# Kernel optimization log

Measured on AMD Instinct MI355X. Metric: run time of the kernel, lower is better.

Reference implementation:

```python
import jax, jax.numpy as jnp
import numpy as np

B, N, T, W, H, ED, S, C, E = 16, 256, 64, 12, 64, 64, 5, 4, 2048
ALPHA = 1.0
FG = W + H  # gcn_in_channels = window_size + tgcn_hidden_dim


def setup_inputs() -> dict:
    key = jax.random.key(0)
    ks = jax.random.split(key, 26)
    rn = lambda k, shape: jax.random.normal(k, shape, jnp.float32) * 0.1
    x = jax.random.normal(ks[0], (B, N, T), jnp.float32)
    src = jax.random.randint(ks[1], (E,), 0, N)
    off = jax.random.randint(ks[2], (E,), 1, N)
    dst = (src + off) % N  # no self loops
    return {
        'x': x,
        'static_edge_weight': jax.random.uniform(ks[3], (E,), jnp.float32),
        'gsl_gconv_w': rn(ks[4], (FG, ED)), 'gsl_gconv_b': rn(ks[5], (ED,)),
        'gsl_w1': rn(ks[6], (ED, ED)), 'gsl_b1': rn(ks[7], (ED,)),
        'gsl_w2': rn(ks[8], (ED, ED)), 'gsl_b2': rn(ks[9], (ED,)),
        'wz_c': rn(ks[10], (1, H)), 'bz_c': rn(ks[11], (H,)),
        'wz_l': rn(ks[12], (2 * H, H)), 'bz_l': rn(ks[13], (H,)),
        'wr_c': rn(ks[14], (1, H)), 'br_c': rn(ks[15], (H,)),
        'wr_l': rn(ks[16], (2 * H, H)), 'br_l': rn(ks[17], (H,)),
        'wh_c': rn(ks[18], (1, H)), 'bh_c': rn(ks[19], (H,)),
        'wh_l': rn(ks[20], (2 * H, H)), 'bh_l': rn(ks[21], (H,)),
        'cls_w': rn(ks[22], (N * H, C)), 'cls_b': rn(ks[23], (C,)),
        'static_edge_index': jnp.stack([src, dst]).astype(jnp.int32),
    }


def _normalize(A):
    # GCN sym-norm with added self loops; A has zero diagonal by construction.
    Ahat = A + jnp.eye(N, dtype=A.dtype)
    deg = Ahat.sum(axis=-2)  # in-degree (PyG gcn_norm scatters weight on col)
    dinv = jnp.where(deg > 0, 1.0 / jnp.sqrt(deg), 0.0)
    return dinv[..., :, None] * Ahat * dinv[..., None, :]


def reference(x, static_edge_weight, gsl_gconv_w, gsl_gconv_b, gsl_w1, gsl_b1,
              gsl_w2, gsl_b2, wz_c, bz_c, wz_l, bz_l, wr_c, br_c, wr_l, br_l,
              wh_c, bh_c, wh_l, bh_l, cls_w, cls_b, static_edge_index):
    A_stat = jnp.zeros((N, N), jnp.float32).at[static_edge_index[0], static_edge_index[1]].add(static_edge_weight)
    An_stat = _normalize(A_stat)  # [N,N]

    # Sliding windows, left-padded with zeros to window_size W.
    xp = jnp.pad(x, ((0, 0), (0, 0), (W - 1, 0)))
    widx = jnp.arange(T)[:, None] + jnp.arange(W)[None, :]
    wins = jnp.transpose(xp[:, :, widx], (2, 0, 1, 3))      # [T,B,N,W]
    xts = jnp.transpose(x, (2, 0, 1))[..., None]            # [T,B,N,1]
    cnts = jnp.minimum(jnp.arange(T) + 1, S).astype(jnp.float32)
    idxs = jnp.arange(T) % S

    def gcn_s(X, Wm, b):  # static graph, out[j] = sum_i Anorm[i,j] (XW)[i]
        return jnp.einsum('ij,bif->bjf', An_stat, X @ Wm) + b

    def gcn_d(An, X, Wm, b):  # per-batch dynamic graph
        return jnp.einsum('bij,bif->bjf', An, X @ Wm) + b

    def step(carry, xs):
        h, Eh = carry
        win, xt, cnt, idx = xs
        It = jnp.concatenate([win, h], axis=-1)             # [B,N,W+H]
        df = gcn_s(It, gsl_gconv_w, gsl_gconv_b)
        de1 = jnp.tanh(ALPHA * (df @ gsl_w1 + gsl_b1))
        de2 = jnp.tanh(ALPHA * (df @ gsl_w2 + gsl_b2))
        M12 = jnp.einsum('bie,bje->bij', de1, de2)          # de1 @ de2^T
        Et = jax.nn.relu(jnp.tanh(ALPHA * (M12 - jnp.swapaxes(M12, -1, -2))))
        Eh = Eh.at[:, idx].set(Et)                          # ring buffer write
        Mt = Eh.sum(axis=1) / cnt                           # mean over filled slots
        An = _normalize(Mt)
        cz = gcn_d(An, xt, wz_c, bz_c)
        z = jax.nn.sigmoid(jnp.concatenate([cz, h], -1) @ wz_l + bz_l)
        cr = gcn_d(An, xt, wr_c, br_c)
        r = jax.nn.sigmoid(jnp.concatenate([cr, h], -1) @ wr_l + br_l)
        ch = gcn_d(An, xt, wh_c, bh_c)
        ht = jnp.tanh(jnp.concatenate([ch, h * r], -1) @ wh_l + bh_l)
        h = z * h + (1.0 - z) * ht
        return (h, Eh), None

    h0 = jnp.zeros((B, N, H), jnp.float32)
    Eh0 = jnp.zeros((B, S, N, N), jnp.float32)
    (hT, _), _ = jax.lax.scan(step, (h0, Eh0), (wins, xts, cnts, idxs))
    return hT.reshape(B, N * H) @ cls_w + cls_b
```

## Files before the change

kernel.cpp:

```cpp
#include <hip/hip_runtime.h>
#include <hip/hip_bf16.h>


typedef unsigned short u16;
typedef unsigned int u32;
typedef unsigned long long u64;
typedef __attribute__((ext_vector_type(8))) short bf16x8;
typedef __attribute__((ext_vector_type(4))) float f32x4;

#define B_ 16
#define N_ 256
#define T_ 64
#define W_ 12
#define S_ 5
#define E_ 2048
#define FG_ 76
#define G_ 16

__device__ __forceinline__ float b2f(u16 u) {
  union { u32 i; float f; } v; v.i = ((u32)u) << 16; return v.f;
}
__device__ __forceinline__ u16 f2b(float f) {
  union { float f; u32 i; } v; v.f = f;
  u32 x = v.i; x += 0x7fff + ((x >> 16) & 1); return (u16)(x >> 16);
}
__device__ __forceinline__ float ftanh(float x) {
  float e = __expf(-2.f * fabsf(x));
  float t = (1.f - e) / (1.f + e);
  return x < 0.f ? -t : t;
}
__device__ __forceinline__ float fsigm(float x) { return 1.f / (1.f + __expf(-x)); }
__device__ __forceinline__ float cvload(const void* p, int i, int f) {
  return f ? ((const float*)p)[i] : b2f(((const u16*)p)[i]);
}
__device__ __forceinline__ float gld(const float* p) {
  return __hip_atomic_load(p, __ATOMIC_RELAXED, __HIP_MEMORY_SCOPE_SYSTEM);
}
__device__ __forceinline__ void gst(float* p, float v) {
  __hip_atomic_store(p, v, __ATOMIC_RELAXED, __HIP_MEMORY_SCOPE_SYSTEM);
}
__device__ __forceinline__ u64 gld64(const u64* p) {
  return __hip_atomic_load(p, __ATOMIC_RELAXED, __HIP_MEMORY_SCOPE_SYSTEM);
}
__device__ __forceinline__ void gst64(u64* p, u64 v) {
  __hip_atomic_store(p, v, __ATOMIC_RELAXED, __HIP_MEMORY_SCOPE_SYSTEM);
}
__device__ __forceinline__ u32 gldu(const u32* p) {
  return __hip_atomic_load(p, __ATOMIC_RELAXED, __HIP_MEMORY_SCOPE_SYSTEM);
}
__device__ __forceinline__ f32x4 mfma16(bf16x8 a, bf16x8 b, f32x4 c) {
  return __builtin_amdgcn_mfma_f32_16x16x32_bf16(a, b, c, 0, 0, 0);
}
__device__ __forceinline__ bf16x8 ldfrag(const u16* p) { return *(const bf16x8*)p; }

struct Params {
  const void *x0, *ew0, *gw0, *gb0, *w10, *b10, *w20, *b20;
  const void *wzc0, *bzc0, *wzl0, *bzl0, *wrc0, *brc0, *wrl0, *brl0;
  const void *whc0, *bhc0, *whl0, *bhl0, *clsw0, *clsb0;
  const int* eidx;
  float *xf, *ewf, *gwf, *gbf, *b1f, *b2ff;
  float *wzcf, *bzcf, *wzlf, *bzlf, *wrcf, *brcf, *wrlf, *brlf;
  float *whcf, *bhcf, *whlf, *bhlf, *clswf, *clsbf;
  u16 *w1h, *w2h;
  float *AnT, *dinvS, *uvF, *h, *degsum, *Eh, *Ascr;
  u64 *de1g, *de2g, *xTp, *hgpT;
  u32 *tags;
  int *flag;
  void* out;
};

__device__ __forceinline__ void wtag(const u32* tg, u32 target) {
  const int k = threadIdx.x & 15;
  while (!__all((int)(gldu(&tg[k]) >= target)))
    __builtin_amdgcn_s_sleep(1);
}
__device__ __forceinline__ void ptag(u32* tg, int wg, u32 val) {
  if (threadIdx.x == 0)
    __hip_atomic_store(&tg[wg], val, __ATOMIC_RELAXED, __HIP_MEMORY_SCOPE_SYSTEM);
}

__global__ void k_detect(Params p) {
  if (threadIdx.x == 0) {
    const u16* q = (const u16*)p.x0;
    int c = 0;
    for (int i = 0; i < 256; ++i) {
      int ex = (q[i] >> 7) & 0xff;
      c += (ex >= 110 && ex <= 135);
    }
    *p.flag = (c < 200) ? 1 : 0;
  }
}

__global__ void k_convert(Params p) {
  const int f = *p.flag;
  const int blk = blockIdx.x, tid = threadIdx.x;
  if (blk < 32) {
    const int base = blk * 8192;
    for (int i = tid; i < 8192; i += 256) p.xf[base + i] = cvload(p.x0, base + i, f);
    return;
  }
  if (blk == 51) { for (int i = tid; i < 4096; i += 256) p.w1h[i] = f ? f2b(((const float*)p.w10)[i]) : ((const u16*)p.w10)[i]; return; }
  if (blk == 52) { for (int i = tid; i < 4096; i += 256) p.w2h[i] = f ? f2b(((const float*)p.w20)[i]) : ((const u16*)p.w20)[i]; return; }
  const void* src = nullptr; float* dst = nullptr; int n = 0;
  switch (blk) {
    case 32: src = p.ew0;  dst = p.ewf;  n = E_;      break;
    case 33: src = p.gw0;  dst = p.gwf;  n = FG_ * 64; break;
    case 34: src = p.gb0;  dst = p.gbf;  n = 64;      break;
    case 35: src = p.b10;  dst = p.b1f;  n = 64;      break;
    case 36: src = p.b20;  dst = p.b2ff; n = 64;      break;
    case 37: src = p.wzc0; dst = p.wzcf; n = 64;      break;
    case 38: src = p.bzc0; dst = p.bzcf; n = 64;      break;
    case 39: src = p.wzl0; dst = p.wzlf; n = 8192;    break;
    case 40: src = p.bzl0; dst = p.bzlf; n = 64;      break;
    case 41: src = p.wrc0; dst = p.wrcf; n = 64;      break;
    case 42: src = p.brc0; dst = p.brcf; n = 64;      break;
    case 43: src = p.wrl0; dst = p.wrlf; n = 8192;    break;
    case 44: src = p.brl0; dst = p.brlf; n = 64;      break;
    case 45: src = p.whc0; dst = p.whcf; n = 64;      break;
    case 46: src = p.bhc0; dst = p.bhcf; n = 64;      break;
    case 47: src = p.whl0; dst = p.whlf; n = 8192;    break;
    case 48: src = p.bhl0; dst = p.bhlf; n = 64;      break;
    case 49: src = p.clsw0; dst = p.clswf; n = 65536; break;
    case 50: src = p.clsb0; dst = p.clsbf; n = 4;     break;
    default: return;
  }
  for (int i = tid; i < n; i += 256) dst[i] = cvload(src, i, f);
}

__global__ void k_xt(Params p) {
  __shared__ float tile[64 * 65];
  const int b = blockIdx.x, tid = threadIdx.x;
  u32* xT32 = (u32*)p.xTp;
  for (int chunk = 0; chunk < 4; ++chunk) {
    __syncthreads();
    const int r = tid >> 2, tq = (tid & 3) * 16;
    #pragma unroll
    for (int q = 0; q < 16; ++q)
      tile[r * 65 + tq + q] = p.xf[((size_t)b * N_ + chunk * 64 + r) * T_ + tq + q];
    __syncthreads();
    #pragma unroll
    for (int q = 0; q < 8; ++q) {
      const int idx = q * 256 + tid;
      const int t = idx >> 5, c = idx & 31;
      u32 v = (u32)f2b(tile[(2 * c) * 65 + t]) | ((u32)f2b(tile[(2 * c + 1) * 65 + t]) << 16);
      xT32[(size_t)(b * 64 + t) * 128 + chunk * 32 + c] = v;
    }
  }
}

__global__ void k_scatter(Params p) {
  for (int e = threadIdx.x; e < E_; e += 256) {
    int s = p.eidx[e], d = p.eidx[E_ + e];
    atomicAdd(&p.Ascr[s * N_ + d], p.ewf[e]);
  }
}
__global__ void k_deg(Params p) {
  int j = threadIdx.x;
  float dg = 1.f;
  for (int i = 0; i < N_; ++i) dg += p.Ascr[i * N_ + j];
  p.dinvS[j] = rsqrtf(dg);
}
__global__ void k_ant(Params p) {
  int i = blockIdx.x, j = threadIdx.x;
  float a = p.Ascr[i * N_ + j] + (i == j ? 1.f : 0.f);
  p.AnT[j * N_ + i] = p.dinvS[i] * a * p.dinvS[j];
}
__global__ void k_uv(Params p) {
  int e = threadIdx.x; if (e >= 64) return;
  float uz = 0, vz = 0, ur = 0, vr = 0, uh = 0, vh = 0;
  for (int f = 0; f < 64; ++f) {
    float wz = p.wzlf[f * 64 + e], wr = p.wrlf[f * 64 + e], wh = p.whlf[f * 64 + e];
    uz += p.wzcf[f] * wz; vz += p.bzcf[f] * wz;
    ur += p.wrcf[f] * wr; vr += p.brcf[f] * wr;
    uh += p.whcf[f] * wh; vh += p.bhcf[f] * wh;
  }
  p.uvF[0 * 64 + e] = uz; p.uvF[1 * 64 + e] = vz + p.bzlf[e];
  p.uvF[2 * 64 + e] = ur; p.uvF[3 * 64 + e] = vr + p.brlf[e];
  p.uvF[4 * 64 + e] = uh; p.uvF[5 * 64 + e] = vh + p.bhlf[e];
}

__global__ void __launch_bounds__(256) dtgcn_main(Params p) {
  __shared__ __align__(16) u16 s_union[21120];
  __shared__ __align__(16) u16 s_gwF[64 * 104];
  __shared__ __align__(16) u16 s_w1T[64 * 72], s_w2T[64 * 72];
  __shared__ __align__(16) u16 s_gzT[64 * 72], s_grT[64 * 72], s_ghT[64 * 72];
  __shared__ __align__(16) u16 s_antO1[16 * 264], s_antO2[16 * 264];
  __shared__ __align__(16) u16 s_m1[16 * 104];
  __shared__ float s_msum[16 * 257];
  __shared__ __align__(16) u16 s_de1I[16 * 72], s_de2I[16 * 72];
  __shared__ __align__(16) u16 s_hbf[16 * 72];
  __shared__ __align__(16) u16 s_dfhr[16 * 72];
  __shared__ float s_colv[16], s_degacc[16];
  __shared__ float s_y[256], s_dinv[256], s_s[16];
  __shared__ float s_uv[384], s_gb[64], s_b1[64], s_b2[64];

  const int b = blockIdx.x & 15;
  const int wg = blockIdx.x >> 4;
  const int tid = threadIdx.x;
  const int lane = tid & 63;
  const int wv = tid >> 6;
  const int l = lane & 15;
  const int quad = lane >> 4;
  const int r0 = wg * 16;

  for (int idx = tid; idx < 64 * 104; idx += 256) {
    const int ee = idx / 104, k = idx - ee * 104;
    u16 v = 0;
    if (k < 64) v = f2b(p.gwf[(12 + k) * 64 + ee]);
    else if (k < 76) v = f2b(p.gwf[(k - 64) * 64 + ee]);
    s_gwF[ee * 104 + k] = v;
  }
  for (int idx = tid; idx < 4096; idx += 256) {
    const int ee = idx >> 6, ff = idx & 63;
    s_w1T[ee * 72 + ff] = p.w1h[ff * 64 + ee];
    s_w2T[ee * 72 + ff] = p.w2h[ff * 64 + ee];
    s_gzT[ee * 72 + ff] = f2b(p.wzlf[4096 + ff * 64 + ee]);
    s_grT[ee * 72 + ff] = f2b(p.wrlf[4096 + ff * 64 + ee]);
    s_ghT[ee * 72 + ff] = f2b(p.whlf[4096 + ff * 64 + ee]);
    const int j = idx >> 8, i = idx & 255;
    float a = p.AnT[(r0 + j) * N_ + i];
    u16 hi = f2b(a);
    s_antO1[j * 264 + i] = hi;
    s_antO2[j * 264 + i] = f2b(a - b2f(hi));
  }
  for (int idx = tid; idx < 16 * 257; idx += 256) s_msum[idx] = 0.f;
  for (int idx = tid; idx < 16 * 72; idx += 256) s_hbf[idx] = 0;
  for (int idx = tid; idx < 16 * 104; idx += 256) s_m1[idx] = 0;
  for (int idx = 20064 + tid; idx < 21120; idx += 256) s_union[idx] = 0;
  for (int idx = tid; idx < 384; idx += 256) s_uv[idx] = p.uvF[idx];
  if (tid < 64) { s_gb[tid] = p.gbf[tid]; s_b1[tid] = p.b1f[tid]; s_b2[tid] = p.b2ff[tid]; }
  if (tid < 16) s_degacc[tid] = 0.f;
  __syncthreads();

  u64* de1g = p.de1g + (size_t)b * N_ * 16;
  u64* de2g = p.de2g + (size_t)b * N_ * 16;
  u64* hgpb = p.hgpT + (size_t)b * 64 * 64;
  const u64* xTb = p.xTp + (size_t)b * 64 * 64;
  float* hb   = p.h + (size_t)b * N_ * 64;
  float* degb = p.degsum + (size_t)b * N_;
  u32* tgDe = p.tags + b * 64;
  u32* tgDg = p.tags + b * 64 + 16;
  u32* tgH  = p.tags + b * 64 + 32;

  u16* s_itT = s_union;
  u16* s_j1  = s_union;
  u16* s_j2  = s_union + 9216;
  float* s_part = (float*)s_union;

  float hreg[4] = {0.f, 0.f, 0.f, 0.f};
  const int e = wv * 16 + l;

  for (int t = 0; t < T_; ++t) {
    {
      u64 tw[3];
      #pragma unroll
      for (int q = 0; q < 3; ++q) {
        const int idx = q * 256 + tid;
        const int row = idx >> 6, c = idx & 63;
        const int tx = t - (W_ - 1) + row;
        tw[q] = (tx >= 0) ? gld64(&xTb[(size_t)tx * 64 + c]) : 0ull;
      }
      wtag(tgH, (u32)t);
      u64 th[16];
      #pragma unroll
      for (int q = 0; q < 16; ++q) {
        const int idx = q * 256 + tid;
        const int row = idx >> 6, c = idx & 63;
        th[q] = gld64(&hgpb[(size_t)row * 64 + c]);
      }
      #pragma unroll
      for (int q = 0; q < 16; ++q) {
        const int idx = q * 256 + tid;
        const int row = idx >> 6, c = idx & 63;
        *(u64*)&s_itT[row * 264 + c * 4] = th[q];
      }
      #pragma unroll
      for (int q = 0; q < 3; ++q) {
        const int idx = q * 256 + tid;
        const int row = idx >> 6, c = idx & 63;
        *(u64*)&s_itT[(64 + row) * 264 + c * 4] = tw[q];
      }
      __syncthreads();
      for (int nt = wv; nt < 5; nt += 4) {
        f32x4 acc = {0.f, 0.f, 0.f, 0.f};
        #pragma unroll
        for (int ch = 0; ch < 8; ++ch) {
          const int io = ch * 32 + quad * 8;
          bf16x8 bfr = ldfrag(&s_itT[(nt * 16 + l) * 264 + io]);
          acc = mfma16(ldfrag(&s_antO1[l * 264 + io]), bfr, acc);
          acc = mfma16(ldfrag(&s_antO2[l * 264 + io]), bfr, acc);
        }
        #pragma unroll
        for (int r = 0; r < 4; ++r)
          s_m1[(quad * 4 + r) * 104 + nt * 16 + l] = f2b(acc[r]);
      }
      __syncthreads();
      {
        f32x4 dfa = {0.f, 0.f, 0.f, 0.f};
        #pragma unroll
        for (int ks = 0; ks < 3; ++ks) {
          bf16x8 afr = ldfrag(&s_m1[l * 104 + ks * 32 + quad * 8]);
          dfa = mfma16(afr, ldfrag(&s_gwF[e * 104 + ks * 32 + quad * 8]), dfa);
        }
        #pragma unroll
        for (int r = 0; r < 4; ++r)
          s_dfhr[(quad * 4 + r) * 72 + e] = f2b(dfa[r] + s_gb[e]);
      }
      __syncthreads();
      {
        f32x4 E1, E2;
        #pragma unroll
        for (int r = 0; r < 4; ++r) { E1[r] = s_b1[e]; E2[r] = s_b2[e]; }
        #pragma unroll
        for (int ks = 0; ks < 2; ++ks) {
          bf16x8 afr = ldfrag(&s_dfhr[l * 72 + ks * 32 + quad * 8]);
          E1 = mfma16(afr, ldfrag(&s_w1T[e * 72 + ks * 32 + quad * 8]), E1);
          E2 = mfma16(afr, ldfrag(&s_w2T[e * 72 + ks * 32 + quad * 8]), E2);
        }
        #pragma unroll
        for (int r = 0; r < 4; ++r) {
          s_de1I[(quad * 4 + r) * 72 + e] = f2b(ftanh(E1[r]));
          s_de2I[(quad * 4 + r) * 72 + e] = f2b(ftanh(E2[r]));
        }
      }
      __syncthreads();
      {
        const int row = tid >> 4, c = tid & 15;
        u64 v1 = *(const u64*)&s_de1I[row * 72 + c * 4];
        u64 v2 = *(const u64*)&s_de2I[row * 72 + c * 4];
        gst64(&de1g[(size_t)(r0 + row) * 16 + c], v1);
        gst64(&de2g[(size_t)(r0 + row) * 16 + c], v2);
      }
      __syncthreads();
      ptag(tgDe, wg, (u32)(t + 1));
    }

    {
      const int sidx = t % S_;
      float* Ehc = p.Eh + (size_t)(b * S_ + sidx) * N_ * N_;
      if (tid < 16) s_colv[tid] = 0.f;
      bf16x8 bq1[2], bq2[2];
      #pragma unroll
      for (int ks = 0; ks < 2; ++ks) {
        bq1[ks] = ldfrag(&s_de1I[l * 72 + ks * 32 + quad * 8]);
        bq2[ks] = ldfrag(&s_de2I[l * 72 + ks * 32 + quad * 8]);
      }
      wtag(tgDe, (u32)(t + 1));
      float dcacc = 0.f;
      for (int jh = 0; jh < 2; ++jh) {
        u64 t1[8], t2[8];
        #pragma unroll
        for (int q = 0; q < 8; ++q) {
          const int idx = q * 256 + tid;
          const int row = idx >> 4, c = idx & 15;
          t1[q] = gld64(&de1g[(size_t)(jh * 128 + row) * 16 + c]);
          t2[q] = gld64(&de2g[(size_t)(jh * 128 + row) * 16 + c]);
        }
        __syncthreads();
        #pragma unroll
        for (int q = 0; q < 8; ++q) {
          const int idx = q * 256 + tid;
          const int row = idx >> 4, c = idx & 15;
          *(u64*)&s_j1[row * 72 + c * 4] = t1[q];
          *(u64*)&s_j2[row * 72 + c * 4] = t2[q];
        }
        __syncthreads();
        #pragma unroll
        for (int mt2 = 0; mt2 < 2; ++mt2) {
          const int mt = wv * 2 + mt2;
          f32x4 D1 = {0.f, 0.f, 0.f, 0.f}, D2 = {0.f, 0.f, 0.f, 0.f};
          #pragma unroll
          for (int ks = 0; ks < 2; ++ks) {
            bf16x8 a1 = ldfrag(&s_j1[(mt * 16 + l) * 72 + ks * 32 + quad * 8]);
            bf16x8 a2 = ldfrag(&s_j2[(mt * 16 + l) * 72 + ks * 32 + quad * 8]);
            D1 = mfma16(a1, bq2[ks], D1);
            D2 = mfma16(a2, bq1[ks], D2);
          }
          #pragma unroll
          for (int r = 0; r < 4; ++r) {
            const int i = jh * 128 + mt * 16 + quad * 4 + r;
            float d = ftanh(D1[r] - D2[r]);
            float eN = fmaxf(d, 0.f);
            float old = Ehc[(r0 + l) * N_ + i];
            float dd = eN - old;
            Ehc[(r0 + l) * N_ + i] = eN;
            s_msum[l * 257 + i] += dd;
            dcacc += dd;
          }
        }
      }
      dcacc += __shfl_xor(dcacc, 16);
      dcacc += __shfl_xor(dcacc, 32);
      if (lane < 16) atomicAdd(&s_colv[lane], dcacc);
      __syncthreads();
      if (tid < 16) {
        float nd = s_degacc[tid] + s_colv[tid];
        s_degacc[tid] = nd;
        gst(&degb[r0 + tid], nd);
      }
      __syncthreads();
      ptag(tgDg, wg, (u32)(t + 1));
    }

    {
      f32x4 azh = {0.f, 0.f, 0.f, 0.f}, arh = {0.f, 0.f, 0.f, 0.f};
      #pragma unroll
      for (int ks = 0; ks < 2; ++ks) {
        bf16x8 afr = ldfrag(&s_hbf[l * 72 + ks * 32 + quad * 8]);
        azh = mfma16(afr, ldfrag(&s_gzT[e * 72 + ks * 32 + quad * 8]), azh);
        arh = mfma16(afr, ldfrag(&s_grT[e * 72 + ks * 32 + quad * 8]), arh);
      }
      wtag(tgDg, (u32)(t + 1));
      const float cnt = (float)((t + 1 < S_) ? (t + 1) : S_);
      const float invc = 1.f / cnt;
      {
        float dg = 1.f + gld(&degb[tid]) * invc;
        float di = rsqrtf(dg);
        float xv = p.xf[((size_t)b * N_ + tid) * T_ + t];
        s_dinv[tid] = di;
        s_y[tid] = di * xv;
      }
      __syncthreads();
      {
        const int jl = tid & 15, c = tid >> 4;
        float part = 0.f;
        #pragma unroll
        for (int k = 0; k < 16; ++k)
          part += s_msum[jl * 257 + c * 16 + k] * s_y[c * 16 + k];
        s_part[c * 16 + jl] = part;
      }
      __syncthreads();
      if (tid < 16) {
        float tot = 0.f;
        for (int k = 0; k < 16; ++k) tot += s_part[k * 16 + tid];
        const int j = r0 + tid;
        s_s[tid] = s_dinv[j] * (tot * invc + s_y[j]);
      }
      __syncthreads();
      float sv[4];
      #pragma unroll
      for (int r = 0; r < 4; ++r) sv[r] = s_s[quad * 4 + r];
      float zz[4], rr2[4];
      #pragma unroll
      for (int r = 0; r < 4; ++r) {
        zz[r]  = fsigm(azh[r] + s_uv[0 * 64 + e] * sv[r] + s_uv[1 * 64 + e]);
        rr2[r] = fsigm(arh[r] + s_uv[2 * 64 + e] * sv[r] + s_uv[3 * 64 + e]);
      }
      #pragma unroll
      for (int r = 0; r < 4; ++r)
        s_dfhr[(quad * 4 + r) * 72 + e] = f2b(hreg[r] * rr2[r]);
      __syncthreads();
      f32x4 ah;
      #pragma unroll
      for (int r = 0; r < 4; ++r) ah[r] = s_uv[4 * 64 + e] * sv[r] + s_uv[5 * 64 + e];
      #pragma unroll
      for (int ks = 0; ks < 2; ++ks) {
        bf16x8 afr = ldfrag(&s_dfhr[l * 72 + ks * 32 + quad * 8]);
        ah = mfma16(afr, ldfrag(&s_ghT[e * 72 + ks * 32 + quad * 8]), ah);
      }
      #pragma unroll
      for (int r = 0; r < 4; ++r) {
        float ht = ftanh(ah[r]);
        hreg[r] = zz[r] * hreg[r] + (1.f - zz[r]) * ht;
      }
      #pragma unroll
      for (int r = 0; r < 4; ++r)
        s_hbf[(quad * 4 + r) * 72 + e] = f2b(hreg[r]);
      if (t == T_ - 1) {
        #pragma unroll
        for (int r = 0; r < 4; ++r)
          hb[(r0 + quad * 4 + r) * 64 + e] = hreg[r];
      }
      __syncthreads();
      {
        const int k = tid >> 2, c4 = tid & 3;
        u64 v = (u64)s_hbf[(c4 * 4 + 0) * 72 + k]
              | ((u64)s_hbf[(c4 * 4 + 1) * 72 + k] << 16)
              | ((u64)s_hbf[(c4 * 4 + 2) * 72 + k] << 32)
              | ((u64)s_hbf[(c4 * 4 + 3) * 72 + k] << 48);
        gst64(&hgpb[(size_t)k * 64 + (r0 >> 2) + c4], v);
      }
      __syncthreads();
      ptag(tgH, wg, (u32)(t + 1));
    }
  }
}

__global__ void k_cls(Params p) {
  __shared__ float red[256][4];
  const int b = blockIdx.x, i = threadIdx.x;
  const float* hr = p.h + ((size_t)b * N_ + i) * 64;
  const float* w = p.clswf + (size_t)i * 64 * 4;
  float a0 = 0, a1 = 0, a2 = 0, a3 = 0;
  for (int f = 0; f < 64; ++f) {
    float hv = hr[f];
    a0 += hv * w[f * 4 + 0]; a1 += hv * w[f * 4 + 1];
    a2 += hv * w[f * 4 + 2]; a3 += hv * w[f * 4 + 3];
  }
  red[i][0] = a0; red[i][1] = a1; red[i][2] = a2; red[i][3] = a3;
  __syncthreads();
  for (int st = 128; st > 0; st >>= 1) {
    if (i < st) {
      red[i][0] += red[i + st][0]; red[i][1] += red[i + st][1];
      red[i][2] += red[i + st][2]; red[i][3] += red[i + st][3];
    }
    __syncthreads();
  }
  if (i < 4) {
    float v = red[0][i] + p.clsbf[i];
    if (*p.flag) ((float*)p.out)[b * 4 + i] = v;
    else         ((u16*)p.out)[b * 4 + i] = f2b(v);
  }
}

extern "C" void kernel_launch(void* const* d_in, const int* in_sizes, int n_in,
                              void* d_out, int out_size, void* d_ws, size_t ws_size,
                              hipStream_t stream) {
  float* w = (float*)d_ws;
  size_t o = 0;
  auto alloc = [&](size_t n) { float* r = w + o; o += (n + 63) & ~(size_t)63; return r; };
  float* xf    = alloc(262144);
  float* ewf   = alloc(E_);
  float* gwf   = alloc(FG_ * 64);
  float* gbf   = alloc(64);
  float* b1f   = alloc(64);
  float* b2ff  = alloc(64);
  float* wzcf  = alloc(64); float* bzcf = alloc(64); float* wzlf = alloc(8192); float* bzlf = alloc(64);
  float* wrcf  = alloc(64); float* brcf = alloc(64); float* wrlf = alloc(8192); float* brlf = alloc(64);
  float* whcf  = alloc(64); float* bhcf = alloc(64); float* whlf = alloc(8192); float* bhlf = alloc(64);
  float* clswf = alloc(65536); float* clsbf = alloc(64);
  u16* w1h = (u16*)alloc(2048);
  u16* w2h = (u16*)alloc(2048);
  int* flag = (int*)alloc(64);
  float* AnT   = alloc(65536);
  float* dinvS = alloc(256);
  float* uvF   = alloc(384);
  u64* de1g = (u64*)alloc((size_t)B_ * N_ * 32);
  u64* de2g = (u64*)alloc((size_t)B_ * N_ * 32);
  u64* xTp  = (u64*)alloc((size_t)B_ * 64 * 128);
  const size_t zero_off = o;
  float* Ascr  = alloc((size_t)N_ * N_);
  float* h     = alloc((size_t)B_ * N_ * 64);
  u64*   hgpT  = (u64*)alloc((size_t)B_ * 64 * 128);
  float* degs  = alloc((size_t)B_ * N_);
  u32*   tags  = (u32*)alloc(B_ * 64);
  float* Eh    = alloc((size_t)B_ * S_ * N_ * N_);
  if (ws_size < o * sizeof(float)) return;

  (void)hipMemsetAsync(w + zero_off, 0, (o - zero_off) * sizeof(float), stream);

  Params p;
  p.x0  = d_in[0];  p.ew0 = d_in[1];
  p.gw0 = d_in[2];  p.gb0 = d_in[3];
  p.w10 = d_in[4];  p.b10 = d_in[5];
  p.w20 = d_in[6];  p.b20 = d_in[7];
  p.wzc0 = d_in[8];  p.bzc0 = d_in[9];  p.wzl0 = d_in[10]; p.bzl0 = d_in[11];
  p.wrc0 = d_in[12]; p.brc0 = d_in[13]; p.wrl0 = d_in[14]; p.brl0 = d_in[15];
  p.whc0 = d_in[16]; p.bhc0 = d_in[17]; p.whl0 = d_in[18]; p.bhl0 = d_in[19];
  p.clsw0 = d_in[20]; p.clsb0 = d_in[21];
  p.eidx = (const int*)d_in[22];
  p.xf = xf; p.ewf = ewf; p.gwf = gwf; p.gbf = gbf; p.b1f = b1f; p.b2ff = b2ff;
  p.wzcf = wzcf; p.bzcf = bzcf; p.wzlf = wzlf; p.bzlf = bzlf;
  p.wrcf = wrcf; p.brcf = brcf; p.wrlf = wrlf; p.brlf = brlf;
  p.whcf = whcf; p.bhcf = bhcf; p.whlf = whlf; p.bhlf = bhlf;
  p.clswf = clswf; p.clsbf = clsbf; p.w1h = w1h; p.w2h = w2h;
  p.AnT = AnT; p.dinvS = dinvS; p.uvF = uvF;
  p.h = h; p.degsum = degs; p.Eh = Eh; p.Ascr = Ascr;
  p.de1g = de1g; p.de2g = de2g; p.xTp = xTp; p.hgpT = hgpT;
  p.tags = tags; p.flag = flag; p.out = d_out;

  k_detect<<<1, 64, 0, stream>>>(p);
  k_convert<<<53, 256, 0, stream>>>(p);
  k_xt<<<B_, 256, 0, stream>>>(p);
  k_scatter<<<1, 256, 0, stream>>>(p);
  k_deg<<<1, 256, 0, stream>>>(p);
  k_ant<<<N_, 256, 0, stream>>>(p);
  k_uv<<<1, 64, 0, stream>>>(p);

  void* args[] = { &p };
  hipError_t ce = hipLaunchCooperativeKernel((const void*)dtgcn_main,
                                             dim3(B_ * G_), dim3(256), args, 0, stream);
  if (ce != hipSuccess) {
    (void)hipGetLastError();
    dtgcn_main<<<dim3(B_ * G_), dim3(256), 0, stream>>>(p);
  }

  k_cls<<<B_, 256, 0, stream>>>(p);
}
```

Before: 950.7 us.

## Fold preprocessing and classifier into persistent kernel, split h-exchange waits by halves

Removes the separate detect, convert, transpose, scatter, degree, normalization, uv and classifier kernels and performs that work inside the cooperative main kernel, with each workgroup building its own normalized adjacency slice and converting weights directly from the inputs. The final classifier becomes a per-workgroup partial reduction combined through tagged global partials. The per-step hidden-state exchange now waits separately on two halves of the producer workgroups, so MFMA work on the first half of the node dimension can start before the second half is published. This cuts launch overhead and intermediate buffers but duplicates the edge scatter in every workgroup and adds extra synchronisation tags.

```diff
diff --git a/kernel.cpp b/kernel.cpp
--- a/kernel.cpp
+++ b/kernel.cpp
@@ -14,7 +14,6 @@
 #define W_ 12
 #define S_ 5
 #define E_ 2048
-#define FG_ 76
 #define G_ 16
 
 __device__ __forceinline__ float b2f(u16 u) {
@@ -30,8 +29,11 @@
   return x < 0.f ? -t : t;
 }
 __device__ __forceinline__ float fsigm(float x) { return 1.f / (1.f + __expf(-x)); }
-__device__ __forceinline__ float cvload(const void* p, int i, int f) {
+__device__ __forceinline__ float cvload(const void* p, size_t i, int f) {
   return f ? ((const float*)p)[i] : b2f(((const u16*)p)[i]);
+}
+__device__ __forceinline__ u16 cvloadb(const void* p, size_t i, int f) {
+  return f ? f2b(((const float*)p)[i]) : ((const u16*)p)[i];
 }
 __device__ __forceinline__ float gld(const float* p) {
   return __hip_atomic_load(p, __ATOMIC_RELAXED, __HIP_MEMORY_SCOPE_SYSTEM);
@@ -58,14 +60,9 @@
   const void *wzc0, *bzc0, *wzl0, *bzl0, *wrc0, *brc0, *wrl0, *brl0;
   const void *whc0, *bhc0, *whl0, *bhl0, *clsw0, *clsb0;
   const int* eidx;
-  float *xf, *ewf, *gwf, *gbf, *b1f, *b2ff;
-  float *wzcf, *bzcf, *wzlf, *bzlf, *wrcf, *brcf, *wrlf, *brlf;
-  float *whcf, *bhcf, *whlf, *bhlf, *clswf, *clsbf;
-  u16 *w1h, *w2h;
-  float *AnT, *dinvS, *uvF, *h, *degsum, *Eh, *Ascr;
+  float *degsum, *Eh, *clspart;
   u64 *de1g, *de2g, *xTp, *hgpT;
   u32 *tags;
-  int *flag;
   void* out;
 };
 
@@ -74,109 +71,14 @@
   while (!__all((int)(gldu(&tg[k]) >= target)))
     __builtin_amdgcn_s_sleep(1);
 }
+__device__ __forceinline__ void wtag8(const u32* tg, int base, u32 target) {
+  const int k = base + (threadIdx.x & 7);
+  while (!__all((int)(gldu(&tg[k]) >= target)))
+    __builtin_amdgcn_s_sleep(1);
+}
 __device__ __forceinline__ void ptag(u32* tg, int wg, u32 val) {
   if (threadIdx.x == 0)
     __hip_atomic_store(&tg[wg], val, __ATOMIC_RELAXED, __HIP_MEMORY_SCOPE_SYSTEM);
-}
-
-__global__ void k_detect(Params p) {
-  if (threadIdx.x == 0) {
-    const u16* q = (const u16*)p.x0;
-    int c = 0;
-    for (int i = 0; i < 256; ++i) {
-      int ex = (q[i] >> 7) & 0xff;
-      c += (ex >= 110 && ex <= 135);
-    }
-    *p.flag = (c < 200) ? 1 : 0;
-  }
-}
-
-__global__ void k_convert(Params p) {
-  const int f = *p.flag;
-  const int blk = blockIdx.x, tid = threadIdx.x;
-  if (blk < 32) {
-    const int base = blk * 8192;
-    for (int i = tid; i < 8192; i += 256) p.xf[base + i] = cvload(p.x0, base + i, f);
-    return;
-  }
-  if (blk == 51) { for (int i = tid; i < 4096; i += 256) p.w1h[i] = f ? f2b(((const float*)p.w10)[i]) : ((const u16*)p.w10)[i]; return; }
-  if (blk == 52) { for (int i = tid; i < 4096; i += 256) p.w2h[i] = f ? f2b(((const float*)p.w20)[i]) : ((const u16*)p.w20)[i]; return; }
-  const void* src = nullptr; float* dst = nullptr; int n = 0;
-  switch (blk) {
-    case 32: src = p.ew0;  dst = p.ewf;  n = E_;      break;
-    case 33: src = p.gw0;  dst = p.gwf;  n = FG_ * 64; break;
-    case 34: src = p.gb0;  dst = p.gbf;  n = 64;      break;
-    case 35: src = p.b10;  dst = p.b1f;  n = 64;      break;
-    case 36: src = p.b20;  dst = p.b2ff; n = 64;      break;
-    case 37: src = p.wzc0; dst = p.wzcf; n = 64;      break;
-    case 38: src = p.bzc0; dst = p.bzcf; n = 64;      break;
-    case 39: src = p.wzl0; dst = p.wzlf; n = 8192;    break;
-    case 40: src = p.bzl0; dst = p.bzlf; n = 64;      break;
-    case 41: src = p.wrc0; dst = p.wrcf; n = 64;      break;
-    case 42: src = p.brc0; dst = p.brcf; n = 64;      break;
-    case 43: src = p.wrl0; dst = p.wrlf; n = 8192;    break;
-    case 44: src = p.brl0; dst = p.brlf; n = 64;      break;
-    case 45: src = p.whc0; dst = p.whcf; n = 64;      break;
-    case 46: src = p.bhc0; dst = p.bhcf; n = 64;      break;
-    case 47: src = p.whl0; dst = p.whlf; n = 8192;    break;
-    case 48: src = p.bhl0; dst = p.bhlf; n = 64;      break;
-    case 49: src = p.clsw0; dst = p.clswf; n = 65536; break;
-    case 50: src = p.clsb0; dst = p.clsbf; n = 4;     break;
-    default: return;
-  }
-  for (int i = tid; i < n; i += 256) dst[i] = cvload(src, i, f);
-}
-
-__global__ void k_xt(Params p) {
-  __shared__ float tile[64 * 65];
-  const int b = blockIdx.x, tid = threadIdx.x;
-  u32* xT32 = (u32*)p.xTp;
-  for (int chunk = 0; chunk < 4; ++chunk) {
-    __syncthreads();
-    const int r = tid >> 2, tq = (tid & 3) * 16;
-    #pragma unroll
-    for (int q = 0; q < 16; ++q)
-      tile[r * 65 + tq + q] = p.xf[((size_t)b * N_ + chunk * 64 + r) * T_ + tq + q];
-    __syncthreads();
-    #pragma unroll
-    for (int q = 0; q < 8; ++q) {
-      const int idx = q * 256 + tid;
-      const int t = idx >> 5, c = idx & 31;
-      u32 v = (u32)f2b(tile[(2 * c) * 65 + t]) | ((u32)f2b(tile[(2 * c + 1) * 65 + t]) << 16);
-      xT32[(size_t)(b * 64 + t) * 128 + chunk * 32 + c] = v;
-    }
-  }
-}
-
-__global__ void k_scatter(Params p) {
-  for (int e = threadIdx.x; e < E_; e += 256) {
-    int s = p.eidx[e], d = p.eidx[E_ + e];
-    atomicAdd(&p.Ascr[s * N_ + d], p.ewf[e]);
-  }
-}
-__global__ void k_deg(Params p) {
-  int j = threadIdx.x;
-  float dg = 1.f;
-  for (int i = 0; i < N_; ++i) dg += p.Ascr[i * N_ + j];
-  p.dinvS[j] = rsqrtf(dg);
-}
-__global__ void k_ant(Params p) {
-  int i = blockIdx.x, j = threadIdx.x;
-  float a = p.Ascr[i * N_ + j] + (i == j ? 1.f : 0.f);
-  p.AnT[j * N_ + i] = p.dinvS[i] * a * p.dinvS[j];
-}
-__global__ void k_uv(Params p) {
-  int e = threadIdx.x; if (e >= 64) return;
-  float uz = 0, vz = 0, ur = 0, vr = 0, uh = 0, vh = 0;
-  for (int f = 0; f < 64; ++f) {
-    float wz = p.wzlf[f * 64 + e], wr = p.wrlf[f * 64 + e], wh = p.whlf[f * 64 + e];
-    uz += p.wzcf[f] * wz; vz += p.bzcf[f] * wz;
-    ur += p.wrcf[f] * wr; vr += p.brcf[f] * wr;
-    uh += p.whcf[f] * wh; vh += p.bhcf[f] * wh;
-  }
-  p.uvF[0 * 64 + e] = uz; p.uvF[1 * 64 + e] = vz + p.bzlf[e];
-  p.uvF[2 * 64 + e] = ur; p.uvF[3 * 64 + e] = vr + p.brlf[e];
-  p.uvF[4 * 64 + e] = uh; p.uvF[5 * 64 + e] = vh + p.bhlf[e];
 }
 
 __global__ void __launch_bounds__(256) dtgcn_main(Params p) {
@@ -193,6 +95,7 @@
   __shared__ float s_colv[16], s_degacc[16];
   __shared__ float s_y[256], s_dinv[256], s_s[16];
   __shared__ float s_uv[384], s_gb[64], s_b1[64], s_b2[64];
+  __shared__ int s_flag;
 
   const int b = blockIdx.x & 15;
   const int wg = blockIdx.x >> 4;
@@ -203,44 +106,113 @@
   const int quad = lane >> 4;
   const int r0 = wg * 16;
 
+  u64* de1g = p.de1g + (size_t)b * N_ * 16;
+  u64* de2g = p.de2g + (size_t)b * N_ * 16;
+  u64* hgpb = p.hgpT + (size_t)b * 64 * 64;
+  u64* xTw  = p.xTp + (size_t)b * 64 * 64;
+  const u64* xTb = xTw;
+  float* degb = p.degsum + (size_t)b * N_;
+  u32* tgDe = p.tags + b * 128;
+  u32* tgDg = p.tags + b * 128 + 16;
+  u32* tgH  = p.tags + b * 128 + 32;
+  u32* tgX  = p.tags + b * 128 + 48;
+  u32* tgC  = p.tags + b * 128 + 64;
+
+  if (tid == 0) {
+    const u16* q = (const u16*)p.x0;
+    int c = 0;
+    for (int i = 0; i < 256; ++i) {
+      int ex = (q[i] >> 7) & 0xff;
+      c += (ex >= 110 && ex <= 135);
+    }
+    s_flag = (c < 200) ? 1 : 0;
+  }
+  __syncthreads();
+  const int fl = s_flag;
+
+  {
+    u16* xs = s_union;
+    #pragma unroll
+    for (int r = 0; r < 4; ++r) {
+      const int tt = wg * 4 + r;
+      xs[r * 256 + tid] = f2b(cvload(p.x0, ((size_t)b * N_ + tid) * T_ + tt, fl));
+    }
+    __syncthreads();
+    const int r = tid >> 6, c = tid & 63;
+    u64 v = (u64)xs[r * 256 + 4 * c]
+          | ((u64)xs[r * 256 + 4 * c + 1] << 16)
+          | ((u64)xs[r * 256 + 4 * c + 2] << 32)
+          | ((u64)xs[r * 256 + 4 * c + 3] << 48);
+    gst64(&xTw[(size_t)(wg * 4 + r) * 64 + c], v);
+    __syncthreads();
+    ptag(tgX, wg, 1);
+  }
+
+  {
+    float* s_acol = (float*)s_union;
+    float* s_dg   = (float*)s_union + 4096;
+    for (int i = tid; i < 4096; i += 256) s_acol[i] = 0.f;
+    s_dg[tid] = 0.f;
+    __syncthreads();
+    for (int e2 = tid; e2 < E_; e2 += 256) {
+      const int sN = p.eidx[e2], dN = p.eidx[E_ + e2];
+      const float wv2 = cvload(p.ew0, e2, fl);
+      atomicAdd(&s_dg[dN], wv2);
+      const int dl = dN - r0;
+      if (dl >= 0 && dl < 16) atomicAdd(&s_acol[sN * 16 + dl], wv2);
+    }
+    __syncthreads();
+    s_dg[tid] = rsqrtf(1.f + s_dg[tid]);
+    __syncthreads();
+    for (int idx = tid; idx < 4096; idx += 256) {
+      const int jl = idx >> 8, i = idx & 255;
+      float a = s_acol[i * 16 + jl] + ((i == r0 + jl) ? 1.f : 0.f);
+      float v = s_dg[i] * a * s_dg[r0 + jl];
+      u16 hi = f2b(v);
+      s_antO1[jl * 264 + i] = hi;
+      s_antO2[jl * 264 + i] = f2b(v - b2f(hi));
+    }
+  }
+
   for (int idx = tid; idx < 64 * 104; idx += 256) {
     const int ee = idx / 104, k = idx - ee * 104;
     u16 v = 0;
-    if (k < 64) v = f2b(p.gwf[(12 + k) * 64 + ee]);
-    else if (k < 76) v = f2b(p.gwf[(k - 64) * 64 + ee]);
+    if (k < 64) v = cvloadb(p.gw0, (12 + k) * 64 + ee, fl);
+    else if (k < 76) v = cvloadb(p.gw0, (k - 64) * 64 + ee, fl);
     s_gwF[ee * 104 + k] = v;
   }
   for (int idx = tid; idx < 4096; idx += 256) {
     const int ee = idx >> 6, ff = idx & 63;
-    s_w1T[ee * 72 + ff] = p.w1h[ff * 64 + ee];
-    s_w2T[ee * 72 + ff] = p.w2h[ff * 64 + ee];
-    s_gzT[ee * 72 + ff] = f2b(p.wzlf[4096 + ff * 64 + ee]);
-    s_grT[ee * 72 + ff] = f2b(p.wrlf[4096 + ff * 64 + ee]);
-    s_ghT[ee * 72 + ff] = f2b(p.whlf[4096 + ff * 64 + ee]);
-    const int j = idx >> 8, i = idx & 255;
-    float a = p.AnT[(r0 + j) * N_ + i];
-    u16 hi = f2b(a);
-    s_antO1[j * 264 + i] = hi;
-    s_antO2[j * 264 + i] = f2b(a - b2f(hi));
+    s_w1T[ee * 72 + ff] = cvloadb(p.w10, ff * 64 + ee, fl);
+    s_w2T[ee * 72 + ff] = cvloadb(p.w20, ff * 64 + ee, fl);
+    s_gzT[ee * 72 + ff] = cvloadb(p.wzl0, 4096 + ff * 64 + ee, fl);
+    s_grT[ee * 72 + ff] = cvloadb(p.wrl0, 4096 + ff * 64 + ee, fl);
+    s_ghT[ee * 72 + ff] = cvloadb(p.whl0, 4096 + ff * 64 + ee, fl);
+  }
+  if (tid < 64) {
+    const int e2 = tid;
+    float uz = 0, vz = 0, ur = 0, vr = 0, uh = 0, vh = 0;
+    for (int f = 0; f < 64; ++f) {
+      float wz = cvload(p.wzl0, f * 64 + e2, fl);
+      float wr = cvload(p.wrl0, f * 64 + e2, fl);
+      float wh = cvload(p.whl0, f * 64 + e2, fl);
+      uz += cvload(p.wzc0, f, fl) * wz; vz += cvload(p.bzc0, f, fl) * wz;
+      ur += cvload(p.wrc0, f, fl) * wr; vr += cvload(p.brc0, f, fl) * wr;
+      uh += cvload(p.whc0, f, fl) * wh; vh += cvload(p.bhc0, f, fl) * wh;
+    }
+    s_uv[0 * 64 + e2] = uz; s_uv[1 * 64 + e2] = vz + cvload(p.bzl0, e2, fl);
+    s_uv[2 * 64 + e2] = ur; s_uv[3 * 64 + e2] = vr + cvload(p.brl0, e2, fl);
+    s_uv[4 * 64 + e2] = uh; s_uv[5 * 64 + e2] = vh + cvload(p.bhl0, e2, fl);
+    s_gb[tid] = cvload(p.gb0, tid, fl);
+    s_b1[tid] = cvload(p.b10, tid, fl);
+    s_b2[tid] = cvload(p.b20, tid, fl);
   }
   for (int idx = tid; idx < 16 * 257; idx += 256) s_msum[idx] = 0.f;
   for (int idx = tid; idx < 16 * 72; idx += 256) s_hbf[idx] = 0;
   for (int idx = tid; idx < 16 * 104; idx += 256) s_m1[idx] = 0;
   for (int idx = 20064 + tid; idx < 21120; idx += 256) s_union[idx] = 0;
-  for (int idx = tid; idx < 384; idx += 256) s_uv[idx] = p.uvF[idx];
-  if (tid < 64) { s_gb[tid] = p.gbf[tid]; s_b1[tid] = p.b1f[tid]; s_b2[tid] = p.b2ff[tid]; }
   if (tid < 16) s_degacc[tid] = 0.f;
   __syncthreads();
-
-  u64* de1g = p.de1g + (size_t)b * N_ * 16;
-  u64* de2g = p.de2g + (size_t)b * N_ * 16;
-  u64* hgpb = p.hgpT + (size_t)b * 64 * 64;
-  const u64* xTb = p.xTp + (size_t)b * 64 * 64;
-  float* hb   = p.h + (size_t)b * N_ * 64;
-  float* degb = p.degsum + (size_t)b * N_;
-  u32* tgDe = p.tags + b * 64;
-  u32* tgDg = p.tags + b * 64 + 16;
-  u32* tgH  = p.tags + b * 64 + 32;
 
   u16* s_itT = s_union;
   u16* s_j1  = s_union;
@@ -252,47 +224,98 @@
 
   for (int t = 0; t < T_; ++t) {
     {
-      u64 tw[3];
-      #pragma unroll
-      for (int q = 0; q < 3; ++q) {
+      if (t == 0) wtag(tgX, 1);
+      u64 tw0[2], tw1[2];
+      #pragma unroll
+      for (int q = 0; q < 2; ++q) {
         const int idx = q * 256 + tid;
-        const int row = idx >> 6, c = idx & 63;
+        const int row = idx >> 5, c = idx & 31;
+        const bool ok = idx < 384;
         const int tx = t - (W_ - 1) + row;
-        tw[q] = (tx >= 0) ? gld64(&xTb[(size_t)tx * 64 + c]) : 0ull;
-      }
-      wtag(tgH, (u32)t);
-      u64 th[16];
-      #pragma unroll
-      for (int q = 0; q < 16; ++q) {
-        const int idx = q * 256 + tid;
-        const int row = idx >> 6, c = idx & 63;
-        th[q] = gld64(&hgpb[(size_t)row * 64 + c]);
-      }
-      #pragma unroll
-      for (int q = 0; q < 16; ++q) {
-        const int idx = q * 256 + tid;
-        const int row = idx >> 6, c = idx & 63;
-        *(u64*)&s_itT[row * 264 + c * 4] = th[q];
-      }
-      #pragma unroll
-      for (int q = 0; q < 3; ++q) {
-        const int idx = q * 256 + tid;
-        const int row = idx >> 6, c = idx & 63;
-        *(u64*)&s_itT[(64 + row) * 264 + c * 4] = tw[q];
-      }
-      __syncthreads();
-      for (int nt = wv; nt < 5; nt += 4) {
-        f32x4 acc = {0.f, 0.f, 0.f, 0.f};
-        #pragma unroll
-        for (int ch = 0; ch < 8; ++ch) {
-          const int io = ch * 32 + quad * 8;
-          bf16x8 bfr = ldfrag(&s_itT[(nt * 16 + l) * 264 + io]);
-          acc = mfma16(ldfrag(&s_antO1[l * 264 + io]), bfr, acc);
-          acc = mfma16(ldfrag(&s_antO2[l * 264 + io]), bfr, acc);
-        }
-        #pragma unroll
-        for (int r = 0; r < 4; ++r)
-          s_m1[(quad * 4 + r) * 104 + nt * 16 + l] = f2b(acc[r]);
+        const bool live = ok && tx >= 0;
+        tw0[q] = live ? gld64(&xTb[(size_t)tx * 64 + c]) : 0ull;
+        tw1[q] = live ? gld64(&xTb[(size_t)tx * 64 + 32 + c]) : 0ull;
+      }
+      f32x4 accA[2];
+      accA[0] = (f32x4){0.f, 0.f, 0.f, 0.f};
+      accA[1] = (f32x4){0.f, 0.f, 0.f, 0.f};
+      wtag8(tgH, 0, (u32)t);
+      {
+        u64 th[8];
+        #pragma unroll
+        for (int q = 0; q < 8; ++q) {
+          const int idx = q * 256 + tid;
+          const int row = idx >> 5, c = idx & 31;
+          th[q] = gld64(&hgpb[(size_t)row * 64 + c]);
+        }
+        #pragma unroll
+        for (int q = 0; q < 8; ++q) {
+          const int idx = q * 256 + tid;
+          const int row = idx >> 5, c = idx & 31;
+          *(u64*)&s_itT[row * 264 + c * 4] = th[q];
+        }
+        #pragma unroll
+        for (int q = 0; q < 2; ++q) {
+          const int idx = q * 256 + tid;
+          if (idx < 384) {
+            const int row = idx >> 5, c = idx & 31;
+            *(u64*)&s_itT[(64 + row) * 264 + c * 4] = tw0[q];
+          }
+        }
+      }
+      __syncthreads();
+      {
+        int ti = 0;
+        for (int nt = wv; nt < 5; nt += 4, ++ti) {
+          #pragma unroll
+          for (int ch = 0; ch < 4; ++ch) {
+            const int io = ch * 32 + quad * 8;
+            bf16x8 bfr = ldfrag(&s_itT[(nt * 16 + l) * 264 + io]);
+            accA[ti] = mfma16(ldfrag(&s_antO1[l * 264 + io]), bfr, accA[ti]);
+            accA[ti] = mfma16(ldfrag(&s_antO2[l * 264 + io]), bfr, accA[ti]);
+          }
+        }
+      }
+      wtag8(tgH, 8, (u32)t);
+      {
+        u64 th[8];
+        #pragma unroll
+        for (int q = 0; q < 8; ++q) {
+          const int idx = q * 256 + tid;
+          const int row = idx >> 5, c = idx & 31;
+          th[q] = gld64(&hgpb[(size_t)row * 64 + 32 + c]);
+        }
+        __syncthreads();
+        #pragma unroll
+        for (int q = 0; q < 8; ++q) {
+          const int idx = q * 256 + tid;
+          const int row = idx >> 5, c = idx & 31;
+          *(u64*)&s_itT[row * 264 + (32 + c) * 4] = th[q];
+        }
+        #pragma unroll
+        for (int q = 0; q < 2; ++q) {
+          const int idx = q * 256 + tid;
+          if (idx < 384) {
+            const int row = idx >> 5, c = idx & 31;
+            *(u64*)&s_itT[(64 + row) * 264 + (32 + c) * 4] = tw1[q];
+          }
+        }
+      }
+      __syncthreads();
+      {
+        int ti = 0;
+        for (int nt = wv; nt < 5; nt += 4, ++ti) {
+          #pragma unroll
+          for (int ch = 4; ch < 8; ++ch) {
+            const int io = ch * 32 + quad * 8;
+            bf16x8 bfr = ldfrag(&s_itT[(nt * 16 + l) * 264 + io]);
+            accA[ti] = mfma16(ldfrag(&s_antO1[l * 264 + io]), bfr, accA[ti]);
+            accA[ti] = mfma16(ldfrag(&s_antO2[l * 264 + io]), bfr, accA[ti]);
+          }
+          #pragma unroll
+          for (int r = 0; r < 4; ++r)
+            s_m1[(quad * 4 + r) * 104 + nt * 16 + l] = f2b(accA[ti][r]);
+        }
       }
       __syncthreads();
       {
@@ -345,9 +368,9 @@
         bq1[ks] = ldfrag(&s_de1I[l * 72 + ks * 32 + quad * 8]);
         bq2[ks] = ldfrag(&s_de2I[l * 72 + ks * 32 + quad * 8]);
       }
-      wtag(tgDe, (u32)(t + 1));
       float dcacc = 0.f;
       for (int jh = 0; jh < 2; ++jh) {
+        wtag8(tgDe, jh * 8, (u32)(t + 1));
         u64 t1[8], t2[8];
         #pragma unroll
         for (int q = 0; q < 8; ++q) {
@@ -416,7 +439,7 @@
       {
         float dg = 1.f + gld(&degb[tid]) * invc;
         float di = rsqrtf(dg);
-        float xv = p.xf[((size_t)b * N_ + tid) * T_ + t];
+        float xv = cvload(p.x0, ((size_t)b * N_ + tid) * T_ + t, fl);
         s_dinv[tid] = di;
         s_y[tid] = di * xv;
       }
@@ -466,11 +489,6 @@
       #pragma unroll
       for (int r = 0; r < 4; ++r)
         s_hbf[(quad * 4 + r) * 72 + e] = f2b(hreg[r]);
-      if (t == T_ - 1) {
-        #pragma unroll
-        for (int r = 0; r < 4; ++r)
-          hb[(r0 + quad * 4 + r) * 64 + e] = hreg[r];
-      }
       __syncthreads();
       {
         const int k = tid >> 2, c4 = tid & 3;
@@ -484,32 +502,41 @@
       ptag(tgH, wg, (u32)(t + 1));
     }
   }
-}
-
-__global__ void k_cls(Params p) {
-  __shared__ float red[256][4];
-  const int b = blockIdx.x, i = threadIdx.x;
-  const float* hr = p.h + ((size_t)b * N_ + i) * 64;
-  const float* w = p.clswf + (size_t)i * 64 * 4;
-  float a0 = 0, a1 = 0, a2 = 0, a3 = 0;
-  for (int f = 0; f < 64; ++f) {
-    float hv = hr[f];
-    a0 += hv * w[f * 4 + 0]; a1 += hv * w[f * 4 + 1];
-    a2 += hv * w[f * 4 + 2]; a3 += hv * w[f * 4 + 3];
-  }
-  red[i][0] = a0; red[i][1] = a1; red[i][2] = a2; red[i][3] = a3;
-  __syncthreads();
-  for (int st = 128; st > 0; st >>= 1) {
-    if (i < st) {
-      red[i][0] += red[i + st][0]; red[i][1] += red[i + st][1];
-      red[i][2] += red[i + st][2]; red[i][3] += red[i + st][3];
-    }
-    __syncthreads();
-  }
-  if (i < 4) {
-    float v = red[0][i] + p.clsbf[i];
-    if (*p.flag) ((float*)p.out)[b * 4 + i] = v;
-    else         ((u16*)p.out)[b * 4 + i] = f2b(v);
+
+  {
+    float part[4] = {0.f, 0.f, 0.f, 0.f};
+    #pragma unroll
+    for (int r = 0; r < 4; ++r) {
+      const size_t base = ((size_t)(r0 + quad * 4 + r) * 64 + e) * 4;
+      #pragma unroll
+      for (int c = 0; c < 4; ++c)
+        part[c] += hreg[r] * cvload(p.clsw0, base + c, fl);
+    }
+    #pragma unroll
+    for (int c = 0; c < 4; ++c) {
+      float v = part[c];
+      v += __shfl_xor(v, 1);  v += __shfl_xor(v, 2);
+      v += __shfl_xor(v, 4);  v += __shfl_xor(v, 8);
+      v += __shfl_xor(v, 16); v += __shfl_xor(v, 32);
+      if (lane == 0) s_s[wv * 4 + c] = v;
+    }
+    __syncthreads();
+    if (tid < 4) {
+      float tot = s_s[0 + tid] + s_s[4 + tid] + s_s[8 + tid] + s_s[12 + tid];
+      gst(&p.clspart[(b * 16 + wg) * 4 + tid], tot);
+    }
+    __syncthreads();
+    ptag(tgC, wg, 1);
+    if (wg == 0) {
+      wtag(tgC, 1);
+      if (tid < 4) {
+        float v = 0.f;
+        for (int k = 0; k < 16; ++k) v += gld(&p.clspart[(b * 16 + k) * 4 + tid]);
+        v += cvload(p.clsb0, tid, fl);
+        if (fl) ((float*)p.out)[b * 4 + tid] = v;
+        else    ((u16*)p.out)[b * 4 + tid] = f2b(v);
+      }
+    }
   }
 }
 
@@ -519,31 +546,14 @@
   float* w = (float*)d_ws;
   size_t o = 0;
   auto alloc = [&](size_t n) { float* r = w + o; o += (n + 63) & ~(size_t)63; return r; };
-  float* xf    = alloc(262144);
-  float* ewf   = alloc(E_);
-  float* gwf   = alloc(FG_ * 64);
-  float* gbf   = alloc(64);
-  float* b1f   = alloc(64);
-  float* b2ff  = alloc(64);
-  float* wzcf  = alloc(64); float* bzcf = alloc(64); float* wzlf = alloc(8192); float* bzlf = alloc(64);
-  float* wrcf  = alloc(64); float* brcf = alloc(64); float* wrlf = alloc(8192); float* brlf = alloc(64);
-  float* whcf  = alloc(64); float* bhcf = alloc(64); float* whlf = alloc(8192); float* bhlf = alloc(64);
-  float* clswf = alloc(65536); float* clsbf = alloc(64);
-  u16* w1h = (u16*)alloc(2048);
-  u16* w2h = (u16*)alloc(2048);
-  int* flag = (int*)alloc(64);
-  float* AnT   = alloc(65536);
-  float* dinvS = alloc(256);
-  float* uvF   = alloc(384);
   u64* de1g = (u64*)alloc((size_t)B_ * N_ * 32);
   u64* de2g = (u64*)alloc((size_t)B_ * N_ * 32);
   u64* xTp  = (u64*)alloc((size_t)B_ * 64 * 128);
+  float* clspart = alloc(B_ * 16 * 4);
   const size_t zero_off = o;
-  float* Ascr  = alloc((size_t)N_ * N_);
-  float* h     = alloc((size_t)B_ * N_ * 64);
   u64*   hgpT  = (u64*)alloc((size_t)B_ * 64 * 128);
   float* degs  = alloc((size_t)B_ * N_);
-  u32*   tags  = (u32*)alloc(B_ * 64);
+  u32*   tags  = (u32*)alloc(B_ * 128);
   float* Eh    = alloc((size_t)B_ * S_ * N_ * N_);
   if (ws_size < o * sizeof(float)) return;
 
@@ -559,23 +569,9 @@
   p.whc0 = d_in[16]; p.bhc0 = d_in[17]; p.whl0 = d_in[18]; p.bhl0 = d_in[19];
   p.clsw0 = d_in[20]; p.clsb0 = d_in[21];
   p.eidx = (const int*)d_in[22];
-  p.xf = xf; p.ewf = ewf; p.gwf = gwf; p.gbf = gbf; p.b1f = b1f; p.b2ff = b2ff;
-  p.wzcf = wzcf; p.bzcf = bzcf; p.wzlf = wzlf; p.bzlf = bzlf;
-  p.wrcf = wrcf; p.brcf = brcf; p.wrlf = wrlf; p.brlf = brlf;
-  p.whcf = whcf; p.bhcf = bhcf; p.whlf = whlf; p.bhlf = bhlf;
-  p.clswf = clswf; p.clsbf = clsbf; p.w1h = w1h; p.w2h = w2h;
-  p.AnT = AnT; p.dinvS = dinvS; p.uvF = uvF;
-  p.h = h; p.degsum = degs; p.Eh = Eh; p.Ascr = Ascr;
+  p.degsum = degs; p.Eh = Eh; p.clspart = clspart;
   p.de1g = de1g; p.de2g = de2g; p.xTp = xTp; p.hgpT = hgpT;
-  p.tags = tags; p.flag = flag; p.out = d_out;
-
-  k_detect<<<1, 64, 0, stream>>>(p);
-  k_convert<<<53, 256, 0, stream>>>(p);
-  k_xt<<<B_, 256, 0, stream>>>(p);
-  k_scatter<<<1, 256, 0, stream>>>(p);
-  k_deg<<<1, 256, 0, stream>>>(p);
-  k_ant<<<N_, 256, 0, stream>>>(p);
-  k_uv<<<1, 64, 0, stream>>>(p);
+  p.tags = tags; p.out = d_out;
 
   void* args[] = { &p };
   hipError_t ce = hipLaunchCooperativeKernel((const void*)dtgcn_main,
@@ -584,6 +580,4 @@
     (void)hipGetLastError();
     dtgcn_main<<<dim3(B_ * G_), dim3(256), 0, stream>>>(p);
   }
-
-  k_cls<<<B_, 256, 0, stream>>>(p);
-}
+}
```

Result: faster. 890.9 us (-6.3%).
